# Performance work log

Hardware: AMD Instinct MI355X
Metric: run time of the kernel (lower is better)

Reference implementation:

```python
import jax, jax.numpy as jnp
import numpy as np

N = 50000   # nodes
E = 800000  # edges
D = 64      # num_filters == hidden_channels
NG = 5      # num_gaussians (edge_attr width, unused by forward math)
NEG_SLOPE = 0.2


def setup_inputs() -> dict:
    key = jax.random.key(0)
    ks = jax.random.split(key, 16)
    s = 1.0 / np.sqrt(D)
    return {
        "x": jax.random.normal(ks[0], (N, D), dtype=jnp.float32),
        "edge_index": jax.random.randint(ks[1], (2, E), 0, N, dtype=jnp.int64),
        "edge_weight": jax.random.uniform(ks[2], (E,), dtype=jnp.float32),
        "edge_attr": jax.random.normal(ks[3], (E, NG), dtype=jnp.float32),
        "W0": jax.random.normal(ks[4], (D, D), dtype=jnp.float32) * s,
        "b0": jnp.zeros((D,), dtype=jnp.float32),
        "W1": jax.random.normal(ks[5], (D, D), dtype=jnp.float32) * s,
        "as1": jax.random.normal(ks[6], (D,), dtype=jnp.float32) * s,
        "ad1": jax.random.normal(ks[7], (D,), dtype=jnp.float32) * s,
        "b1": jnp.zeros((D,), dtype=jnp.float32),
        "W2": jax.random.normal(ks[8], (D, D), dtype=jnp.float32) * s,
        "as2": jax.random.normal(ks[9], (D,), dtype=jnp.float32) * s,
        "ad2": jax.random.normal(ks[10], (D,), dtype=jnp.float32) * s,
        "b2": jnp.zeros((D,), dtype=jnp.float32),
    }


def gat_layer(h, src, dst, W, a_src, a_dst, b):
    # PyG GATConv, heads=1, add_self_loops=False
    hx = h @ W  # [N, D]
    # per-node attention logits, gathered per edge (edge j->i: src=j, dst=i)
    alpha = (hx * a_src).sum(-1)[src] + (hx * a_dst).sum(-1)[dst]  # [E]
    alpha = jax.nn.leaky_relu(alpha, NEG_SLOPE)
    # segment softmax grouped by destination node
    m = jax.ops.segment_max(alpha, dst, num_segments=N)
    e = jnp.exp(alpha - m[dst])
    s = jax.ops.segment_sum(e, dst, num_segments=N)
    p = e / s[dst]  # [E]
    # scatter-add weighted source features
    out = jax.ops.segment_sum(hx[src] * p[:, None], dst, num_segments=N)
    return out + b


def reference(x, edge_index, edge_weight, edge_attr,
              W0, b0, W1, as1, ad1, b1, W2, as2, ad2, b2):
    # edge_weight / edge_attr are accepted but unused, as in the torch module
    src, dst = edge_index[0], edge_index[1]
    out = jax.nn.relu(x @ W0 + b0)
    out = out + jax.nn.relu(gat_layer(out, src, dst, W1, as1, ad1, b1))
    out = out + jax.nn.relu(gat_layer(out, src, dst, W2, as2, ad2, b2))
    return out
```

## Files before the change

### kernel.cpp

```cpp
#include <hip/hip_runtime.h>
#include <hip/hip_bf16.h>

#define DD 64
#define NEG_SLOPE 0.2f
#define HS 68
#define BSH 8
#define BN  256
#define NBMAX 256
#define NBLK 256
#define STAGE_CAP 6144

__device__ __forceinline__ unsigned short f2bf(float f)
{
    unsigned u = __float_as_uint(f);
    u += 0x7FFFu + ((u >> 16) & 1u);
    return (unsigned short)(u >> 16);
}

__global__ __launch_bounds__(256) void k1_count_mm(
    const int4* __restrict__ dst4, const int* __restrict__ dst,
    int* __restrict__ cnts, int NB, int E4, int E, int C4,
    const float* __restrict__ x,
    const float* __restrict__ W0, const float* __restrict__ b0,
    const float* __restrict__ W1,
    const float* __restrict__ a_src, const float* __restrict__ a_dst,
    float* __restrict__ h, ushort4* __restrict__ hxb4,
    float* __restrict__ sarr, float* __restrict__ darr, int n)
{
    __shared__ float Wsh[DD * DD];
    __shared__ float Hsh[DD * HS];
    int tid = threadIdx.x;

    if (blockIdx.x < NBLK) {
        int* lh = (int*)Wsh;
        int k = blockIdx.x;
        for (int i = tid; i < NB; i += 256) lh[i] = 0;
        __syncthreads();
        int i0 = k * C4, i1 = min(i0 + C4, E4);
        for (int i = i0 + tid; i < i1; i += 256) {
            int4 d = dst4[i];
            atomicAdd(&lh[d.x >> BSH], 1);
            atomicAdd(&lh[d.y >> BSH], 1);
            atomicAdd(&lh[d.z >> BSH], 1);
            atomicAdd(&lh[d.w >> BSH], 1);
        }
        if (k == NBLK - 1) {
            for (int e = E4 * 4 + tid; e < E; e += 256)
                atomicAdd(&lh[dst[e] >> BSH], 1);
        }
        __syncthreads();
        for (int i = tid; i < NB; i += 256) cnts[k * NB + i] = lh[i];
        return;
    }

    for (int i = tid * 4; i < DD * DD; i += 1024)
        *(float4*)&Wsh[i] = *(const float4*)&W0[i];

    int fg = tid & 15, ng = tid >> 4;
    int tile0 = (blockIdx.x - NBLK) * 64;
    for (int p = 0; p < 4; ++p) {
        int nl = p * 16 + ng, gn = tile0 + nl;
        if (gn < n)
            *(float4*)&Hsh[nl * HS + 4 * fg] = *(const float4*)&x[gn * DD + 4 * fg];
    }
    __syncthreads();

    float4 acc[4];
#pragma unroll
    for (int j = 0; j < 4; ++j) acc[j] = float4{0.f, 0.f, 0.f, 0.f};
#pragma unroll 8
    for (int k = 0; k < DD; ++k) {
        float4 w4 = *(float4*)&Wsh[k * DD + 4 * fg];
#pragma unroll
        for (int j = 0; j < 4; ++j) {
            float hv = Hsh[(4 * ng + j) * HS + k];
            acc[j].x += hv * w4.x; acc[j].y += hv * w4.y;
            acc[j].z += hv * w4.z; acc[j].w += hv * w4.w;
        }
    }

    float4 b4 = *(const float4*)&b0[4 * fg];
    float4 o[4];
#pragma unroll
    for (int j = 0; j < 4; ++j) {
        o[j].x = fmaxf(acc[j].x + b4.x, 0.f);
        o[j].y = fmaxf(acc[j].y + b4.y, 0.f);
        o[j].z = fmaxf(acc[j].z + b4.z, 0.f);
        o[j].w = fmaxf(acc[j].w + b4.w, 0.f);
        int gn = tile0 + 4 * ng + j;
        if (gn < n) *(float4*)&h[gn * DD + 4 * fg] = o[j];
    }
    __syncthreads();

#pragma unroll
    for (int j = 0; j < 4; ++j)
        *(float4*)&Hsh[(4 * ng + j) * HS + 4 * fg] = o[j];
    for (int i = tid * 4; i < DD * DD; i += 1024)
        *(float4*)&Wsh[i] = *(const float4*)&W1[i];
    __syncthreads();

#pragma unroll
    for (int j = 0; j < 4; ++j) acc[j] = float4{0.f, 0.f, 0.f, 0.f};
#pragma unroll 8
    for (int k = 0; k < DD; ++k) {
        float4 w4 = *(float4*)&Wsh[k * DD + 4 * fg];
#pragma unroll
        for (int j = 0; j < 4; ++j) {
            float hv = Hsh[(4 * ng + j) * HS + k];
            acc[j].x += hv * w4.x; acc[j].y += hv * w4.y;
            acc[j].z += hv * w4.z; acc[j].w += hv * w4.w;
        }
    }

    float4 as4 = *(const float4*)&a_src[4 * fg];
    float4 ad4 = *(const float4*)&a_dst[4 * fg];
#pragma unroll
    for (int j = 0; j < 4; ++j) {
        int gn = tile0 + 4 * ng + j;
        if (gn < n) {
            ushort4 hb;
            hb.x = f2bf(acc[j].x); hb.y = f2bf(acc[j].y);
            hb.z = f2bf(acc[j].z); hb.w = f2bf(acc[j].w);
            hxb4[gn * 16 + fg] = hb;
        }
        float ps = acc[j].x * as4.x + acc[j].y * as4.y + acc[j].z * as4.z + acc[j].w * as4.w;
        float pd = acc[j].x * ad4.x + acc[j].y * ad4.y + acc[j].z * ad4.z + acc[j].w * ad4.w;
#pragma unroll
        for (int off = 8; off; off >>= 1) {
            ps += __shfl_xor(ps, off);
            pd += __shfl_xor(pd, off);
        }
        if (fg == 0 && gn < n) { sarr[gn] = ps; darr[gn] = pd; }
    }
}

__global__ __launch_bounds__(256) void mm_gat(
    const float* __restrict__ h, const float* __restrict__ W,
    const float* __restrict__ a_src, const float* __restrict__ a_dst,
    ushort4* __restrict__ hxb4, float* __restrict__ sarr, float* __restrict__ darr,
    int n)
{
    __shared__ float Wsh[DD * DD];
    __shared__ float Hsh[DD * HS];
    int tid = threadIdx.x;
    for (int i = tid * 4; i < DD * DD; i += 1024)
        *(float4*)&Wsh[i] = *(const float4*)&W[i];

    int fg = tid & 15, ng = tid >> 4;
    int tile0 = blockIdx.x * 64;
    for (int p = 0; p < 4; ++p) {
        int nl = p * 16 + ng, gn = tile0 + nl;
        if (gn < n)
            *(float4*)&Hsh[nl * HS + 4 * fg] = *(const float4*)&h[gn * DD + 4 * fg];
    }
    __syncthreads();

    float4 acc[4];
#pragma unroll
    for (int j = 0; j < 4; ++j) acc[j] = float4{0.f, 0.f, 0.f, 0.f};
#pragma unroll 8
    for (int k = 0; k < DD; ++k) {
        float4 w4 = *(float4*)&Wsh[k * DD + 4 * fg];
#pragma unroll
        for (int j = 0; j < 4; ++j) {
            float hv = Hsh[(4 * ng + j) * HS + k];
            acc[j].x += hv * w4.x; acc[j].y += hv * w4.y;
            acc[j].z += hv * w4.z; acc[j].w += hv * w4.w;
        }
    }

    float4 as4 = *(const float4*)&a_src[4 * fg];
    float4 ad4 = *(const float4*)&a_dst[4 * fg];
#pragma unroll
    for (int j = 0; j < 4; ++j) {
        int gn = tile0 + 4 * ng + j;
        if (gn < n) {
            ushort4 hb;
            hb.x = f2bf(acc[j].x); hb.y = f2bf(acc[j].y);
            hb.z = f2bf(acc[j].z); hb.w = f2bf(acc[j].w);
            hxb4[gn * 16 + fg] = hb;
        }
        float ps = acc[j].x * as4.x + acc[j].y * as4.y + acc[j].z * as4.z + acc[j].w * as4.w;
        float pd = acc[j].x * ad4.x + acc[j].y * ad4.y + acc[j].z * ad4.z + acc[j].w * ad4.w;
#pragma unroll
        for (int off = 8; off; off >>= 1) {
            ps += __shfl_xor(ps, off);
            pd += __shfl_xor(pd, off);
        }
        if (fg == 0 && gn < n) { sarr[gn] = ps; darr[gn] = pd; }
    }
}

__device__ __forceinline__ int wave_incl_scan(int v, int lane)
{
#pragma unroll
    for (int off = 1; off < 64; off <<= 1) {
        int t = __shfl_up(v, off);
        if (lane >= off) v += t;
    }
    return v;
}

__global__ __launch_bounds__(256) void csr_scan(
    const int* __restrict__ cnts, int* __restrict__ boff, int* __restrict__ cbase,
    int* __restrict__ row_ptr, int NB, int N, int E)
{
    __shared__ int wsum[4];
    int t = threadIdx.x, lane = t & 63, w = t >> 6;
    int sum = 0;
    if (t < NB)
        for (int k = 0; k < NBLK; ++k) sum += cnts[k * NB + t];
    int incl = wave_incl_scan(sum, lane);
    if (lane == 63) wsum[w] = incl;
    __syncthreads();
    int wo = 0;
    for (int i = 0; i < w; ++i) wo += wsum[i];
    int excl = wo + incl - sum;
    if (t < NB) {
        boff[t] = excl;
        int run = excl;
        for (int k = 0; k < NBLK; ++k) {
            cbase[k * NB + t] = run;
            run += cnts[k * NB + t];
        }
    }
    if (t == 0) { boff[NB] = E; row_ptr[N] = E; }
}

__global__ __launch_bounds__(512) void chunk_scatter(
    const int4* __restrict__ dst4, const int4* __restrict__ src4,
    const int* __restrict__ dst, const int* __restrict__ src,
    const int* __restrict__ cbase, int* __restrict__ ebuf,
    int NB, int E4, int E, int C4)
{
    __shared__ int lcur[NBMAX];
    int k = blockIdx.x, tid = threadIdx.x;
    for (int i = tid; i < NB; i += 512) lcur[i] = cbase[k * NB + i];
    __syncthreads();
    int i0 = k * C4, i1 = min(i0 + C4, E4);
    for (int i = i0 + tid; i < i1; i += 512) {
        int4 d = dst4[i];
        int4 s = src4[i];
        int b, p;
        b = d.x >> BSH; p = atomicAdd(&lcur[b], 1); ebuf[p] = ((d.x & (BN - 1)) << 24) | s.x;
        b = d.y >> BSH; p = atomicAdd(&lcur[b], 1); ebuf[p] = ((d.y & (BN - 1)) << 24) | s.y;
        b = d.z >> BSH; p = atomicAdd(&lcur[b], 1); ebuf[p] = ((d.z & (BN - 1)) << 24) | s.z;
        b = d.w >> BSH; p = atomicAdd(&lcur[b], 1); ebuf[p] = ((d.w & (BN - 1)) << 24) | s.w;
    }
    if (k == NBLK - 1) {
        for (int e = E4 * 4 + tid; e < E; e += 512) {
            int d = dst[e];
            int b = d >> BSH;
            int p = atomicAdd(&lcur[b], 1);
            ebuf[p] = ((d & (BN - 1)) << 24) | src[e];
        }
    }
}

__global__ __launch_bounds__(512) void group_build(
    const int* __restrict__ ebuf, const int* __restrict__ boff,
    int* __restrict__ row_ptr, int* __restrict__ col, int N)
{
    __shared__ int lcnt[BN];
    __shared__ int loff[BN];
    __shared__ int lcur[BN];
    __shared__ int wsum[4];
    __shared__ int stage[STAGE_CAP];
    int b = blockIdx.x, tid = threadIdx.x;
    int e0 = boff[b], e1 = boff[b + 1];
    int total = e1 - e0;
    if (tid < BN) { lcnt[tid] = 0; lcur[tid] = 0; }
    __syncthreads();
    for (int e = e0 + tid; e < e1; e += 512)
        atomicAdd(&lcnt[((unsigned)ebuf[e]) >> 24], 1);
    __syncthreads();
    int lane = tid & 63, w = tid >> 6;
    int v = (tid < BN) ? lcnt[tid] : 0;
    int incl = wave_incl_scan(v, lane);
    if (tid < BN && lane == 63) wsum[w] = incl;
    __syncthreads();
    if (tid < BN) {
        int wo = 0;
        for (int i = 0; i < w; ++i) wo += wsum[i];
        int excl = wo + incl - v;
        loff[tid] = excl;
        int node = b * BN + tid;
        if (node < N) row_ptr[node] = e0 + excl;
    }
    __syncthreads();
    if (total <= STAGE_CAP) {
        for (int e = e0 + tid; e < e1; e += 512) {
            int p = ebuf[e];
            int dl = ((unsigned)p) >> 24;
            int r = atomicAdd(&lcur[dl], 1);
            stage[loff[dl] + r] = p & 0xFFFFFF;
        }
        __syncthreads();
        for (int i = tid; i < total; i += 512)
            col[e0 + i] = stage[i];
    } else {
        for (int e = e0 + tid; e < e1; e += 512) {
            int p = ebuf[e];
            int dl = ((unsigned)p) >> 24;
            int r = atomicAdd(&lcur[dl], 1);
            col[e0 + loff[dl] + r] = p & 0xFFFFFF;
        }
    }
}

__global__ __launch_bounds__(256) void aggregate(
    const uint4* __restrict__ hxq, const int* __restrict__ row_ptr,
    const int* __restrict__ col, const float* __restrict__ sarr,
    const float* __restrict__ darr, const float* __restrict__ bias,
    float* __restrict__ h, int n)
{
    int tid = threadIdx.x;
    int wid = tid >> 6, lane = tid & 63;
    int fl = lane & 7, es = lane >> 3;
    int v = blockIdx.x * 4 + wid;
    if (v >= n) return;

    int beg = row_ptr[v], end = row_ptr[v + 1];
    float adi = darr[v];
    float m = -3.4e38f, s = 0.f;
    float acc[8];
#pragma unroll
    for (int j = 0; j < 8; ++j) acc[j] = 0.f;

    for (int e = beg + es; e < end; e += 8) {
        int c = col[e];
        float a = sarr[c] + adi;
        a = a > 0.f ? a : NEG_SLOPE * a;
        uint4 u = hxq[c * 8 + fl];
        float mN = fmaxf(m, a);
        float f = __expf(m - mN);
        float wgt = __expf(a - mN);
        m = mN;
        s = s * f + wgt;
        float p0 = __uint_as_float(u.x << 16);
        float p1 = __uint_as_float(u.x & 0xffff0000u);
        float p2 = __uint_as_float(u.y << 16);
        float p3 = __uint_as_float(u.y & 0xffff0000u);
        float p4 = __uint_as_float(u.z << 16);
        float p5 = __uint_as_float(u.z & 0xffff0000u);
        float p6 = __uint_as_float(u.w << 16);
        float p7 = __uint_as_float(u.w & 0xffff0000u);
        acc[0] = acc[0] * f + wgt * p0;
        acc[1] = acc[1] * f + wgt * p1;
        acc[2] = acc[2] * f + wgt * p2;
        acc[3] = acc[3] * f + wgt * p3;
        acc[4] = acc[4] * f + wgt * p4;
        acc[5] = acc[5] * f + wgt * p5;
        acc[6] = acc[6] * f + wgt * p6;
        acc[7] = acc[7] * f + wgt * p7;
    }

#pragma unroll
    for (int off = 8; off < 64; off <<= 1) {
        float m2 = __shfl_xor(m, off);
        float s2 = __shfl_xor(s, off);
        float mN = fmaxf(m, m2);
        float f1 = __expf(m - mN);
        float f2 = __expf(m2 - mN);
        s = s * f1 + s2 * f2;
#pragma unroll
        for (int j = 0; j < 8; ++j) {
            float a2 = __shfl_xor(acc[j], off);
            acc[j] = acc[j] * f1 + a2 * f2;
        }
        m = mN;
    }

    if (es == 0) {
        float inv = (s > 0.f) ? 1.f / s : 0.f;
        float* hp = &h[v * DD + fl * 8];
        float4 c0 = *(float4*)hp;
        float4 c1 = *(float4*)(hp + 4);
        const float* bp = &bias[fl * 8];
        float4 b0 = *(const float4*)bp;
        float4 b1 = *(const float4*)(bp + 4);
        c0.x += fmaxf(acc[0] * inv + b0.x, 0.f);
        c0.y += fmaxf(acc[1] * inv + b0.y, 0.f);
        c0.z += fmaxf(acc[2] * inv + b0.z, 0.f);
        c0.w += fmaxf(acc[3] * inv + b0.w, 0.f);
        c1.x += fmaxf(acc[4] * inv + b1.x, 0.f);
        c1.y += fmaxf(acc[5] * inv + b1.y, 0.f);
        c1.z += fmaxf(acc[6] * inv + b1.z, 0.f);
        c1.w += fmaxf(acc[7] * inv + b1.w, 0.f);
        *(float4*)hp = c0;
        *(float4*)(hp + 4) = c1;
    }
}

extern "C" void kernel_launch(void* const* d_in, const int* in_sizes, int n_in,
                              void* d_out, int out_size, void* d_ws, size_t ws_size,
                              hipStream_t stream)
{
    const float* x  = (const float*)d_in[0];
    const int*   ei = (const int*)d_in[1];
    const float* W0 = (const float*)d_in[4];
    const float* b0 = (const float*)d_in[5];
    const float* W1 = (const float*)d_in[6];
    const float* as1= (const float*)d_in[7];
    const float* ad1= (const float*)d_in[8];
    const float* b1 = (const float*)d_in[9];
    const float* W2 = (const float*)d_in[10];
    const float* as2= (const float*)d_in[11];
    const float* ad2= (const float*)d_in[12];
    const float* b2 = (const float*)d_in[13];

    int N = in_sizes[0] / DD;
    int E = in_sizes[1] / 2;
    int E4 = E >> 2;
    int C4 = (E4 + NBLK - 1) / NBLK;
    int NB = (N + BN - 1) >> BSH;
    float* h = (float*)d_out;

    ushort4* hxb4 = (ushort4*)d_ws;
    float* sarr   = (float*)(hxb4 + (size_t)N * 16);
    float* darr   = sarr + N;
    int*   row_ptr= (int*)(darr + N);
    int*   cnts   = row_ptr + (N + 1);
    int*   cbase  = cnts + NBLK * NB;
    int*   boff   = cbase + NBLK * NB;
    int*   ebuf   = boff + (NB + 1);
    int*   colb   = ebuf + E;

    const int* src = ei;
    const int* dst = ei + E;
    const int4* dst4 = (const int4*)dst;
    const int4* src4 = (const int4*)src;

    int mm_tiles = (N + 63) / 64;
    int agg_blks = (N + 3) / 4;

    k1_count_mm<<<NBLK + mm_tiles, 256, 0, stream>>>(
        dst4, dst, cnts, NB, E4, E, C4,
        x, W0, b0, W1, as1, ad1, h, hxb4, sarr, darr, N);

    csr_scan<<<1, 256, 0, stream>>>(cnts, boff, cbase, row_ptr, NB, N, E);
    chunk_scatter<<<NBLK, 512, 0, stream>>>(dst4, src4, dst, src, cbase, ebuf, NB, E4, E, C4);
    group_build<<<NB, 512, 0, stream>>>(ebuf, boff, row_ptr, colb, N);

    aggregate<<<agg_blks, 256, 0, stream>>>((const uint4*)hxb4, row_ptr, colb, sarr, darr, b1, h, N);

    mm_gat<<<mm_tiles, 256, 0, stream>>>(h, W2, as2, ad2, hxb4, sarr, darr, N);
    aggregate<<<agg_blks, 256, 0, stream>>>((const uint4*)hxb4, row_ptr, colb, sarr, darr, b2, h, N);
}
```

Measured before the change: 219.4 us.

## Fuse CSR scan into scatter, fuse group build with first aggregation, two-pass softmax

Each scatter block now recomputes the per-bucket totals and its own prefix from the count matrix, so the single-block csr_scan launch and the cbase array are gone. The first GAT aggregation is fused into the bucket-grouping kernel, reading column indices straight from shared memory. Nodes with degree up to 64 use a wave-wide two-pass softmax instead of an online rescaling loop. The costs are redundant count reads in every scatter block (256x256) and a lower-parallelism first aggregation (196 blocks of 512 threads each handling 256 nodes).

```diff
diff --git a/kernel.cpp b/kernel.cpp
--- a/kernel.cpp
+++ b/kernel.cpp
@@ -15,6 +15,16 @@
     unsigned u = __float_as_uint(f);
     u += 0x7FFFu + ((u >> 16) & 1u);
     return (unsigned short)(u >> 16);
+}
+
+__device__ __forceinline__ int wave_incl_scan(int v, int lane)
+{
+#pragma unroll
+    for (int off = 1; off < 64; off <<= 1) {
+        int t = __shfl_up(v, off);
+        if (lane >= off) v += t;
+    }
+    return v;
 }
 
 __global__ __launch_bounds__(256) void k1_count_mm(
@@ -191,52 +201,49 @@
     }
 }
 
-__device__ __forceinline__ int wave_incl_scan(int v, int lane)
-{
-#pragma unroll
-    for (int off = 1; off < 64; off <<= 1) {
-        int t = __shfl_up(v, off);
-        if (lane >= off) v += t;
-    }
-    return v;
-}
-
-__global__ __launch_bounds__(256) void csr_scan(
-    const int* __restrict__ cnts, int* __restrict__ boff, int* __restrict__ cbase,
-    int* __restrict__ row_ptr, int NB, int N, int E)
-{
-    __shared__ int wsum[4];
-    int t = threadIdx.x, lane = t & 63, w = t >> 6;
-    int sum = 0;
-    if (t < NB)
-        for (int k = 0; k < NBLK; ++k) sum += cnts[k * NB + t];
-    int incl = wave_incl_scan(sum, lane);
-    if (lane == 63) wsum[w] = incl;
-    __syncthreads();
-    int wo = 0;
-    for (int i = 0; i < w; ++i) wo += wsum[i];
-    int excl = wo + incl - sum;
-    if (t < NB) {
-        boff[t] = excl;
-        int run = excl;
-        for (int k = 0; k < NBLK; ++k) {
-            cbase[k * NB + t] = run;
-            run += cnts[k * NB + t];
-        }
-    }
-    if (t == 0) { boff[NB] = E; row_ptr[N] = E; }
-}
-
-__global__ __launch_bounds__(512) void chunk_scatter(
+__global__ __launch_bounds__(512) void k2_scan_scatter(
+    const int* __restrict__ cnts,
     const int4* __restrict__ dst4, const int4* __restrict__ src4,
     const int* __restrict__ dst, const int* __restrict__ src,
-    const int* __restrict__ cbase, int* __restrict__ ebuf,
-    int NB, int E4, int E, int C4)
+    int* __restrict__ boff, int* __restrict__ row_ptr, int* __restrict__ ebuf,
+    int NB, int N, int E, int E4, int C4)
 {
     __shared__ int lcur[NBMAX];
+    __shared__ int stot[NBMAX];
+    __shared__ int wsum[4];
     int k = blockIdx.x, tid = threadIdx.x;
-    for (int i = tid; i < NB; i += 512) lcur[i] = cbase[k * NB + i];
-    __syncthreads();
+
+    int mybase = 0, tot = 0;
+    if (tid < NB) {
+        for (int kk = 0; kk < NBLK; ++kk) {
+            int c = cnts[kk * NB + tid];
+            tot += c;
+            mybase += (kk < k) ? c : 0;
+        }
+        stot[tid] = tot;
+    }
+    __syncthreads();
+
+    int lane = tid & 63, w = tid >> 6;
+    int incl = 0, v = 0;
+    if (tid < 256) {
+        v = (tid < NB) ? stot[tid] : 0;
+        incl = wave_incl_scan(v, lane);
+        if (lane == 63) wsum[w] = incl;
+    }
+    __syncthreads();
+    if (tid < NB) {
+        int wo = 0;
+        for (int i = 0; i < w; ++i) wo += wsum[i];
+        int excl = wo + incl - v;
+        lcur[tid] = excl + mybase;
+        if (k == 0) {
+            boff[tid] = excl;
+            if (tid == 0) { boff[NB] = E; row_ptr[N] = E; }
+        }
+    }
+    __syncthreads();
+
     int i0 = k * C4, i1 = min(i0 + C4, E4);
     for (int i = i0 + tid; i < i1; i += 512) {
         int4 d = dst4[i];
@@ -257,123 +264,94 @@
     }
 }
 
-__global__ __launch_bounds__(512) void group_build(
-    const int* __restrict__ ebuf, const int* __restrict__ boff,
-    int* __restrict__ row_ptr, int* __restrict__ col, int N)
-{
-    __shared__ int lcnt[BN];
-    __shared__ int loff[BN];
-    __shared__ int lcur[BN];
-    __shared__ int wsum[4];
-    __shared__ int stage[STAGE_CAP];
-    int b = blockIdx.x, tid = threadIdx.x;
-    int e0 = boff[b], e1 = boff[b + 1];
-    int total = e1 - e0;
-    if (tid < BN) { lcnt[tid] = 0; lcur[tid] = 0; }
-    __syncthreads();
-    for (int e = e0 + tid; e < e1; e += 512)
-        atomicAdd(&lcnt[((unsigned)ebuf[e]) >> 24], 1);
-    __syncthreads();
-    int lane = tid & 63, w = tid >> 6;
-    int v = (tid < BN) ? lcnt[tid] : 0;
-    int incl = wave_incl_scan(v, lane);
-    if (tid < BN && lane == 63) wsum[w] = incl;
-    __syncthreads();
-    if (tid < BN) {
-        int wo = 0;
-        for (int i = 0; i < w; ++i) wo += wsum[i];
-        int excl = wo + incl - v;
-        loff[tid] = excl;
-        int node = b * BN + tid;
-        if (node < N) row_ptr[node] = e0 + excl;
-    }
-    __syncthreads();
-    if (total <= STAGE_CAP) {
-        for (int e = e0 + tid; e < e1; e += 512) {
-            int p = ebuf[e];
-            int dl = ((unsigned)p) >> 24;
-            int r = atomicAdd(&lcur[dl], 1);
-            stage[loff[dl] + r] = p & 0xFFFFFF;
-        }
-        __syncthreads();
-        for (int i = tid; i < total; i += 512)
-            col[e0 + i] = stage[i];
-    } else {
-        for (int e = e0 + tid; e < e1; e += 512) {
-            int p = ebuf[e];
-            int dl = ((unsigned)p) >> 24;
-            int r = atomicAdd(&lcur[dl], 1);
-            col[e0 + loff[dl] + r] = p & 0xFFFFFF;
-        }
-    }
-}
-
-__global__ __launch_bounds__(256) void aggregate(
-    const uint4* __restrict__ hxq, const int* __restrict__ row_ptr,
-    const int* __restrict__ col, const float* __restrict__ sarr,
-    const float* __restrict__ darr, const float* __restrict__ bias,
-    float* __restrict__ h, int n)
-{
-    int tid = threadIdx.x;
-    int wid = tid >> 6, lane = tid & 63;
-    int fl = lane & 7, es = lane >> 3;
-    int v = blockIdx.x * 4 + wid;
-    if (v >= n) return;
-
-    int beg = row_ptr[v], end = row_ptr[v + 1];
-    float adi = darr[v];
-    float m = -3.4e38f, s = 0.f;
+__device__ __forceinline__ void agg_node(
+    int node, int deg, const int* colp ,
+    const uint4* __restrict__ hxq, const float* __restrict__ sarr,
+    float adi, const float* __restrict__ bias, float* __restrict__ h,
+    int lane, int fl, int es, bool lds_cols)
+{
     float acc[8];
 #pragma unroll
     for (int j = 0; j < 8; ++j) acc[j] = 0.f;
-
-    for (int e = beg + es; e < end; e += 8) {
-        int c = col[e];
-        float a = sarr[c] + adi;
-        a = a > 0.f ? a : NEG_SLOPE * a;
-        uint4 u = hxq[c * 8 + fl];
-        float mN = fmaxf(m, a);
-        float f = __expf(m - mN);
-        float wgt = __expf(a - mN);
-        m = mN;
-        s = s * f + wgt;
-        float p0 = __uint_as_float(u.x << 16);
-        float p1 = __uint_as_float(u.x & 0xffff0000u);
-        float p2 = __uint_as_float(u.y << 16);
-        float p3 = __uint_as_float(u.y & 0xffff0000u);
-        float p4 = __uint_as_float(u.z << 16);
-        float p5 = __uint_as_float(u.z & 0xffff0000u);
-        float p6 = __uint_as_float(u.w << 16);
-        float p7 = __uint_as_float(u.w & 0xffff0000u);
-        acc[0] = acc[0] * f + wgt * p0;
-        acc[1] = acc[1] * f + wgt * p1;
-        acc[2] = acc[2] * f + wgt * p2;
-        acc[3] = acc[3] * f + wgt * p3;
-        acc[4] = acc[4] * f + wgt * p4;
-        acc[5] = acc[5] * f + wgt * p5;
-        acc[6] = acc[6] * f + wgt * p6;
-        acc[7] = acc[7] * f + wgt * p7;
-    }
-
-#pragma unroll
-    for (int off = 8; off < 64; off <<= 1) {
-        float m2 = __shfl_xor(m, off);
-        float s2 = __shfl_xor(s, off);
-        float mN = fmaxf(m, m2);
-        float f1 = __expf(m - mN);
-        float f2 = __expf(m2 - mN);
-        s = s * f1 + s2 * f2;
-#pragma unroll
-        for (int j = 0; j < 8; ++j) {
-            float a2 = __shfl_xor(acc[j], off);
-            acc[j] = acc[j] * f1 + a2 * f2;
-        }
-        m = mN;
+    float inv = 0.f;
+
+    if (deg > 0 && deg <= 64) {
+        int c = 0; float a = -3.4e38f;
+        if (lane < deg) {
+            c = colp[lane];
+            a = sarr[c] + adi;
+            a = a > 0.f ? a : NEG_SLOPE * a;
+        }
+        float m = a;
+#pragma unroll
+        for (int off = 32; off; off >>= 1) m = fmaxf(m, __shfl_xor(m, off));
+        float wgt = (lane < deg) ? __expf(a - m) : 0.f;
+        float s = wgt;
+#pragma unroll
+        for (int off = 32; off; off >>= 1) s += __shfl_xor(s, off);
+        inv = 1.f / s;
+
+        for (int base = 0; base < deg; base += 8) {
+            int e = base + es;
+            float we = __shfl(wgt, e);
+            int ce = __shfl(c, e);
+            if (we > 0.f) {
+                uint4 u = hxq[(size_t)ce * 8 + fl];
+                acc[0] += we * __uint_as_float(u.x << 16);
+                acc[1] += we * __uint_as_float(u.x & 0xffff0000u);
+                acc[2] += we * __uint_as_float(u.y << 16);
+                acc[3] += we * __uint_as_float(u.y & 0xffff0000u);
+                acc[4] += we * __uint_as_float(u.z << 16);
+                acc[5] += we * __uint_as_float(u.z & 0xffff0000u);
+                acc[6] += we * __uint_as_float(u.w << 16);
+                acc[7] += we * __uint_as_float(u.w & 0xffff0000u);
+            }
+        }
+#pragma unroll
+        for (int off = 8; off < 64; off <<= 1) {
+#pragma unroll
+            for (int j = 0; j < 8; ++j) acc[j] += __shfl_xor(acc[j], off);
+        }
+    } else if (deg > 64) {
+        float m = -3.4e38f, s = 0.f;
+        for (int e = es; e < deg; e += 8) {
+            int cc = colp[e];
+            float a = sarr[cc] + adi;
+            a = a > 0.f ? a : NEG_SLOPE * a;
+            uint4 u = hxq[(size_t)cc * 8 + fl];
+            float mN = fmaxf(m, a);
+            float f = __expf(m - mN);
+            float wg = __expf(a - mN);
+            m = mN; s = s * f + wg;
+            acc[0] = acc[0] * f + wg * __uint_as_float(u.x << 16);
+            acc[1] = acc[1] * f + wg * __uint_as_float(u.x & 0xffff0000u);
+            acc[2] = acc[2] * f + wg * __uint_as_float(u.y << 16);
+            acc[3] = acc[3] * f + wg * __uint_as_float(u.y & 0xffff0000u);
+            acc[4] = acc[4] * f + wg * __uint_as_float(u.z << 16);
+            acc[5] = acc[5] * f + wg * __uint_as_float(u.z & 0xffff0000u);
+            acc[6] = acc[6] * f + wg * __uint_as_float(u.w << 16);
+            acc[7] = acc[7] * f + wg * __uint_as_float(u.w & 0xffff0000u);
+        }
+#pragma unroll
+        for (int off = 8; off < 64; off <<= 1) {
+            float m2 = __shfl_xor(m, off);
+            float s2 = __shfl_xor(s, off);
+            float mN = fmaxf(m, m2);
+            float f1 = __expf(m - mN);
+            float f2 = __expf(m2 - mN);
+            s = s * f1 + s2 * f2;
+#pragma unroll
+            for (int j = 0; j < 8; ++j) {
+                float a2 = __shfl_xor(acc[j], off);
+                acc[j] = acc[j] * f1 + a2 * f2;
+            }
+            m = mN;
+        }
+        inv = (s > 0.f) ? 1.f / s : 0.f;
     }
 
     if (es == 0) {
-        float inv = (s > 0.f) ? 1.f / s : 0.f;
-        float* hp = &h[v * DD + fl * 8];
+        float* hp = &h[(size_t)node * DD + fl * 8];
         float4 c0 = *(float4*)hp;
         float4 c1 = *(float4*)(hp + 4);
         const float* bp = &bias[fl * 8];
@@ -392,6 +370,95 @@
     }
 }
 
+__global__ __launch_bounds__(512) void k3_build_agg(
+    const int* __restrict__ ebuf, const int* __restrict__ boff,
+    int* __restrict__ row_ptr, int* __restrict__ col,
+    const uint4* __restrict__ hxq, const float* __restrict__ sarr,
+    const float* __restrict__ darr, const float* __restrict__ bias,
+    float* __restrict__ h, int N)
+{
+    __shared__ int lcnt[BN];
+    __shared__ int loff[BN + 1];
+    __shared__ int lcur[BN];
+    __shared__ int wsum[4];
+    __shared__ int stage[STAGE_CAP];
+    int b = blockIdx.x, tid = threadIdx.x;
+    int e0 = boff[b], e1 = boff[b + 1];
+    int total = e1 - e0;
+    bool staged = (total <= STAGE_CAP);
+
+    if (tid < BN) { lcnt[tid] = 0; lcur[tid] = 0; }
+    __syncthreads();
+    for (int e = e0 + tid; e < e1; e += 512)
+        atomicAdd(&lcnt[((unsigned)ebuf[e]) >> 24], 1);
+    __syncthreads();
+    int lane = tid & 63, w = tid >> 6;
+    {
+        int v = (tid < BN) ? lcnt[tid] : 0;
+        int incl = wave_incl_scan(v, lane);
+        if (tid < BN && lane == 63) wsum[w] = incl;
+        __syncthreads();
+        if (tid < BN) {
+            int wo = 0;
+            for (int i = 0; i < w; ++i) wo += wsum[i];
+            int excl = wo + incl - v;
+            loff[tid] = excl;
+            int node = b * BN + tid;
+            if (node < N) row_ptr[node] = e0 + excl;
+        }
+        if (tid == 0) loff[BN] = total;
+    }
+    __syncthreads();
+    if (staged) {
+        for (int e = e0 + tid; e < e1; e += 512) {
+            int p = ebuf[e];
+            int dl = ((unsigned)p) >> 24;
+            int r = atomicAdd(&lcur[dl], 1);
+            stage[loff[dl] + r] = p & 0xFFFFFF;
+        }
+        __syncthreads();
+        for (int i = tid; i < total; i += 512)
+            col[e0 + i] = stage[i];
+    } else {
+        for (int e = e0 + tid; e < e1; e += 512) {
+            int p = ebuf[e];
+            int dl = ((unsigned)p) >> 24;
+            int r = atomicAdd(&lcur[dl], 1);
+            col[e0 + loff[dl] + r] = p & 0xFFFFFF;
+        }
+    }
+    __syncthreads();
+
+    int wid = tid >> 6;
+    int fl = lane & 7, es = lane >> 3;
+    for (int it = 0; it < BN / 8; ++it) {
+        int nl = wid * (BN / 8) + it;
+        int node = b * BN + nl;
+        if (node >= N) break;
+        int lbeg = loff[nl];
+        int deg = loff[nl + 1] - lbeg;
+        const int* colp = staged ? &stage[lbeg] : &col[e0 + lbeg];
+        agg_node(node, deg, colp, hxq, sarr, darr[node], bias, h,
+                 lane, fl, es, staged);
+    }
+}
+
+__global__ __launch_bounds__(256) void aggregate2(
+    const uint4* __restrict__ hxq, const int* __restrict__ row_ptr,
+    const int* __restrict__ col, const float* __restrict__ sarr,
+    const float* __restrict__ darr, const float* __restrict__ bias,
+    float* __restrict__ h, int n)
+{
+    int tid = threadIdx.x;
+    int wid = tid >> 6, lane = tid & 63;
+    int fl = lane & 7, es = lane >> 3;
+    int v = blockIdx.x * 4 + wid;
+    if (v >= n) return;
+    int beg = row_ptr[v], end = row_ptr[v + 1];
+    agg_node(v, end - beg, &col[beg], hxq, sarr, darr[v], bias, h,
+             lane, fl, es, false);
+}
+
 extern "C" void kernel_launch(void* const* d_in, const int* in_sizes, int n_in,
                               void* d_out, int out_size, void* d_ws, size_t ws_size,
                               hipStream_t stream)
@@ -421,8 +488,7 @@
     float* darr   = sarr + N;
     int*   row_ptr= (int*)(darr + N);
     int*   cnts   = row_ptr + (N + 1);
-    int*   cbase  = cnts + NBLK * NB;
-    int*   boff   = cbase + NBLK * NB;
+    int*   boff   = cnts + NBLK * NB;
     int*   ebuf   = boff + (NB + 1);
     int*   colb   = ebuf + E;
 
@@ -438,12 +504,13 @@
         dst4, dst, cnts, NB, E4, E, C4,
         x, W0, b0, W1, as1, ad1, h, hxb4, sarr, darr, N);
 
-    csr_scan<<<1, 256, 0, stream>>>(cnts, boff, cbase, row_ptr, NB, N, E);
-    chunk_scatter<<<NBLK, 512, 0, stream>>>(dst4, src4, dst, src, cbase, ebuf, NB, E4, E, C4);
-    group_build<<<NB, 512, 0, stream>>>(ebuf, boff, row_ptr, colb, N);
-
-    aggregate<<<agg_blks, 256, 0, stream>>>((const uint4*)hxb4, row_ptr, colb, sarr, darr, b1, h, N);
+    k2_scan_scatter<<<NBLK, 512, 0, stream>>>(
+        cnts, dst4, src4, dst, src, boff, row_ptr, ebuf, NB, N, E, E4, C4);
+
+    k3_build_agg<<<NB, 512, 0, stream>>>(
+        ebuf, boff, row_ptr, colb, (const uint4*)hxb4, sarr, darr, b1, h, N);
 
     mm_gat<<<mm_tiles, 256, 0, stream>>>(h, W2, as2, ad2, hxb4, sarr, darr, N);
-    aggregate<<<agg_blks, 256, 0, stream>>>((const uint4*)hxb4, row_ptr, colb, sarr, darr, b2, h, N);
-}
+    aggregate2<<<agg_blks, 256, 0, stream>>>(
+        (const uint4*)hxb4, row_ptr, colb, sarr, darr, b2, h, N);
+}
```

After: 274.3 us. 25.0% more time.
